# Optimization experiments

Measured on AMD Instinct MI355X. Metric: run time of the kernel, lower is better.

The kernel has to match this reference:

```python
import jax, jax.numpy as jnp
import numpy as np

BS, M, N = 8, 64, 4096
K_SEL = 32
TEMP = 5.0  # temperature_update_tf(tempIncr=5, epoch=0, n_epochs=2) -> constant at step 0
EPS = 1e-20


def setup_inputs() -> dict:
    key = jax.random.key(0)
    k1, k2 = jax.random.split(key)
    logits = jax.random.normal(k1, (M, N), dtype=jnp.float32)
    u = jax.random.uniform(k2, (BS, M, N), dtype=jnp.float32)
    return {"logits": logits, "u": u}


def reference(logits, u):
    # Gumbel(0, 0.001) noise, exactly as in the TF code
    gn = -0.001 * jnp.log(-jnp.log(u + EPS) + EPS)          # (BS, M, N)
    perturbed = logits[None, :, :] + gn                      # (BS, M, N)
    # tf.nn.top_k(tf.nn.top_k(x, k).indices, k).values then reverse ==
    # top-k indices sorted ascending
    _, idx = jax.lax.top_k(perturbed, K_SEL)                 # (BS, M, k)
    idx_sorted = jnp.sort(idx, axis=-1)
    hard = jax.nn.one_hot(idx_sorted, N, dtype=logits.dtype)  # (BS, M, k, N)
    # exclusive cumsum over the k axis
    cum_mask = jnp.cumsum(hard, axis=-2) - hard               # (BS, M, k, N)
    # log(exp(logits) * (1 - cumMask + eps)) == logits + log(1 - cumMask + eps)
    scores = (logits[None, :, None, :]
              + jnp.log(1.0 - cum_mask + EPS)
              + gn[:, :, None, :]) / TEMP                     # (BS, M, k, N)
    soft = jax.nn.softmax(scores, axis=-1)
    # straight-through: hard forward, soft backward
    return jax.lax.stop_gradient(hard - soft) + soft
```

## Files before the change

### kernel.cpp

```cpp
#include <hip/hip_runtime.h>
#include <math.h>

#define BSZ 8
#define MROWS 64
#define NCOLS 4096
#define KSEL 32
#define EPSF 1e-20f
#define NEG_INF (-3.402823466e+38f)

__global__ __launch_bounds__(256) void topk_onehot_kernel(
    const float* __restrict__ logits,
    const float* __restrict__ u,
    float* __restrict__ out)
{
    __shared__ float vals[4][NCOLS];

    const int r    = blockIdx.x;
    const int m    = r & (MROWS - 1);
    const int tid  = threadIdx.x;
    const int lane = tid & 63;
    const int w    = tid >> 6;

    float* vw = vals[w];

    const float4* u4 = (const float4*)(u + (size_t)r * NCOLS);
    const float4* l4 = (const float4*)(logits + (size_t)m * NCOLS);

    #pragma unroll
    for (int c = 0; c < 16; ++c) {
        int q = (c << 6) + lane;
        float4 uu = u4[q];
        float4 lg = l4[q];
        float px = lg.x - 0.001f * logf(-logf(uu.x + EPSF) + EPSF);
        float py = lg.y - 0.001f * logf(-logf(uu.y + EPSF) + EPSF);
        float pz = lg.z - 0.001f * logf(-logf(uu.z + EPSF) + EPSF);
        float pw = lg.w - 0.001f * logf(-logf(uu.w + EPSF) + EPSF);
        int col   = q << 2;
        int chunk = col >> 6;
        int base  = chunk << 6;
        vw[base + ((col + 0 + chunk) & 63)] = px;
        vw[base + ((col + 1 + chunk) & 63)] = py;
        vw[base + ((col + 2 + chunk) & 63)] = pz;
        vw[base + ((col + 3 + chunk) & 63)] = pw;
    }
    __syncthreads();

    float lmax = NEG_INF;
    int   lidx = 0x7FFFFFFF;
    {
        const int cb = lane << 6;
        #pragma unroll 8
        for (int c = 0; c < 64; ++c) {
            float v = vw[cb + ((c + lane) & 63)];
            if (v > lmax) { lmax = v; lidx = cb + c; }
        }
    }

    unsigned long long removed = 0ull;
    int sel_reg = 0x7FFFFFFF;
    for (int it = 0; it < KSEL; ++it) {
        float bv = lmax; int bi = lidx;
        #pragma unroll
        for (int off = 32; off; off >>= 1) {
            float ov = __shfl_xor(bv, off);
            int   oi = __shfl_xor(bi, off);
            if (ov > bv || (ov == bv && oi < bi)) { bv = ov; bi = oi; }
        }
        if (lane == it) sel_reg = bi;

        const int wl = bi >> 6;
        if (lane == wl) removed |= (1ull << (bi & 63));

        unsigned long long rm = __shfl(removed, wl);
        float nv = vw[(wl << 6) + ((lane + wl) & 63)];
        int   ni = (wl << 6) + lane;
        if ((rm >> lane) & 1ull) nv = NEG_INF;
        #pragma unroll
        for (int off = 32; off; off >>= 1) {
            float ov = __shfl_xor(nv, off);
            int   oi = __shfl_xor(ni, off);
            if (ov > nv || (ov == nv && oi < ni)) { nv = ov; ni = oi; }
        }
        if (lane == wl) { lmax = nv; lidx = ni; }
    }

    int myw = sel_reg;
    int rank = 0;
    #pragma unroll
    for (int j = 0; j < KSEL; ++j) {
        int wj = __shfl(sel_reg, j);
        rank += (wj < myw) ? 1 : 0;
    }
    int* si = (int*)vw;
    if (lane < KSEL) si[rank] = myw;
    __syncthreads();

    #pragma unroll 2
    for (int jj = 0; jj < 8; ++jj) {
        int j  = (w << 3) + jj;
        int t  = si[j];
        int tq = t >> 2;
        int te = t & 3;
        float4* orow = (float4*)(out + (size_t)(r * KSEL + j) * NCOLS);
        #pragma unroll
        for (int c = 0; c < 16; ++c) {
            int q = (c << 6) + lane;
            bool hit = (q == tq);
            float4 z;
            z.x = (hit && te == 0) ? 1.0f : 0.0f;
            z.y = (hit && te == 1) ? 1.0f : 0.0f;
            z.z = (hit && te == 2) ? 1.0f : 0.0f;
            z.w = (hit && te == 3) ? 1.0f : 0.0f;
            orow[q] = z;
        }
    }
}

extern "C" void kernel_launch(void* const* d_in, const int* in_sizes, int n_in,
                              void* d_out, int out_size, void* d_ws, size_t ws_size,
                              hipStream_t stream) {
    const float* logits = (const float*)d_in[0];
    const float* u      = (const float*)d_in[1];
    float* out          = (float*)d_out;

    topk_onehot_kernel<<<BSZ * MROWS, 256, 0, stream>>>(logits, u, out);
}
```

Before: 317.2 us.

## Split top-k selection and one-hot writing into separate kernels

The fused kernel is split into two. The first kernel computes the perturbed row once per block, using all 256 threads for loads, in a single 16 KB shared buffer instead of four redundant per-wave copies, and stores the sorted top-k indices in workspace. The second kernel writes the one-hot output with one wave per output row over many more blocks, so the large store stream is no longer held behind the serial selection loop. This costs an extra launch and a small round trip through global memory, and it assumes the workspace can hold the index buffer.

New measurement: 307.8 us. 1.03x faster.

```diff
diff --git a/kernel.cpp b/kernel.cpp
--- a/kernel.cpp
+++ b/kernel.cpp
@@ -8,27 +8,23 @@
 #define EPSF 1e-20f
 #define NEG_INF (-3.402823466e+38f)
 
-__global__ __launch_bounds__(256) void topk_onehot_kernel(
+__global__ __launch_bounds__(256) void topk_select_kernel(
     const float* __restrict__ logits,
     const float* __restrict__ u,
-    float* __restrict__ out)
+    int* __restrict__ idx_out)
 {
-    __shared__ float vals[4][NCOLS];
+    __shared__ float vals[NCOLS];
 
-    const int r    = blockIdx.x;
-    const int m    = r & (MROWS - 1);
-    const int tid  = threadIdx.x;
-    const int lane = tid & 63;
-    const int w    = tid >> 6;
-
-    float* vw = vals[w];
+    const int r   = blockIdx.x;
+    const int m   = r & (MROWS - 1);
+    const int tid = threadIdx.x;
 
     const float4* u4 = (const float4*)(u + (size_t)r * NCOLS);
     const float4* l4 = (const float4*)(logits + (size_t)m * NCOLS);
 
     #pragma unroll
-    for (int c = 0; c < 16; ++c) {
-        int q = (c << 6) + lane;
+    for (int c = 0; c < 4; ++c) {
+        int q = (c << 8) + tid;
         float4 uu = u4[q];
         float4 lg = l4[q];
         float px = lg.x - 0.001f * logf(-logf(uu.x + EPSF) + EPSF);
@@ -38,12 +34,15 @@
         int col   = q << 2;
         int chunk = col >> 6;
         int base  = chunk << 6;
-        vw[base + ((col + 0 + chunk) & 63)] = px;
-        vw[base + ((col + 1 + chunk) & 63)] = py;
-        vw[base + ((col + 2 + chunk) & 63)] = pz;
-        vw[base + ((col + 3 + chunk) & 63)] = pw;
+        vals[base + ((col + 0 + chunk) & 63)] = px;
+        vals[base + ((col + 1 + chunk) & 63)] = py;
+        vals[base + ((col + 2 + chunk) & 63)] = pz;
+        vals[base + ((col + 3 + chunk) & 63)] = pw;
     }
     __syncthreads();
+
+    if (tid >= 64) return;
+    const int lane = tid;
 
     float lmax = NEG_INF;
     int   lidx = 0x7FFFFFFF;
@@ -51,7 +50,7 @@
         const int cb = lane << 6;
         #pragma unroll 8
         for (int c = 0; c < 64; ++c) {
-            float v = vw[cb + ((c + lane) & 63)];
+            float v = vals[cb + ((c + lane) & 63)];
             if (v > lmax) { lmax = v; lidx = cb + c; }
         }
     }
@@ -72,7 +71,7 @@
         if (lane == wl) removed |= (1ull << (bi & 63));
 
         unsigned long long rm = __shfl(removed, wl);
-        float nv = vw[(wl << 6) + ((lane + wl) & 63)];
+        float nv = vals[(wl << 6) + ((lane + wl) & 63)];
         int   ni = (wl << 6) + lane;
         if ((rm >> lane) & 1ull) nv = NEG_INF;
         #pragma unroll
@@ -91,28 +90,31 @@
         int wj = __shfl(sel_reg, j);
         rank += (wj < myw) ? 1 : 0;
     }
-    int* si = (int*)vw;
-    if (lane < KSEL) si[rank] = myw;
-    __syncthreads();
+    if (lane < KSEL) idx_out[r * KSEL + rank] = myw;
+}
 
-    #pragma unroll 2
-    for (int jj = 0; jj < 8; ++jj) {
-        int j  = (w << 3) + jj;
-        int t  = si[j];
-        int tq = t >> 2;
-        int te = t & 3;
-        float4* orow = (float4*)(out + (size_t)(r * KSEL + j) * NCOLS);
-        #pragma unroll
-        for (int c = 0; c < 16; ++c) {
-            int q = (c << 6) + lane;
-            bool hit = (q == tq);
-            float4 z;
-            z.x = (hit && te == 0) ? 1.0f : 0.0f;
-            z.y = (hit && te == 1) ? 1.0f : 0.0f;
-            z.z = (hit && te == 2) ? 1.0f : 0.0f;
-            z.w = (hit && te == 3) ? 1.0f : 0.0f;
-            orow[q] = z;
-        }
+__global__ __launch_bounds__(256) void onehot_write_kernel(
+    const int* __restrict__ idx,
+    float* __restrict__ out)
+{
+    const int rho  = (blockIdx.x << 2) | (threadIdx.x >> 6);
+    const int lane = threadIdx.x & 63;
+
+    const int t  = idx[rho];
+    const int tq = t >> 2;
+    const int te = t & 3;
+
+    float4* orow = (float4*)(out + (size_t)rho * NCOLS);
+    #pragma unroll
+    for (int c = 0; c < 16; ++c) {
+        int q = (c << 6) + lane;
+        bool hit = (q == tq);
+        float4 z;
+        z.x = (hit && te == 0) ? 1.0f : 0.0f;
+        z.y = (hit && te == 1) ? 1.0f : 0.0f;
+        z.z = (hit && te == 2) ? 1.0f : 0.0f;
+        z.w = (hit && te == 3) ? 1.0f : 0.0f;
+        orow[q] = z;
     }
 }
 
@@ -122,6 +124,8 @@
     const float* logits = (const float*)d_in[0];
     const float* u      = (const float*)d_in[1];
     float* out          = (float*)d_out;
+    int*   idx          = (int*)d_ws;
 
-    topk_onehot_kernel<<<BSZ * MROWS, 256, 0, stream>>>(logits, u, out);
+    topk_select_kernel<<<BSZ * MROWS, 256, 0, stream>>>(logits, u, idx);
+    onehot_write_kernel<<<(BSZ * MROWS * KSEL) / 4, 256, 0, stream>>>(idx, out);
 }
```
